# Kernel optimization log

Measured on AMD Instinct MI355X. Metric: run time of the kernel, lower is better.

## Reference

```python
import jax, jax.numpy as jnp
import numpy as np

BATCH = 8
L = 1024          # sequence length (== init arg l)
DIM = 768         # model dim
HEADS = 12
DIM_HEAD = 64
INNER = HEADS * DIM_HEAD  # 768


def setup_inputs() -> dict:
    key = jax.random.key(0)
    k1, k2, k3, k4 = jax.random.split(key, 4)
    x = jax.random.normal(k1, (BATCH, L, DIM), dtype=jnp.float32)
    # torch nn.Linear stores weight as [out_features, in_features]
    w_qkv = jax.random.normal(k2, (INNER * 3, DIM), dtype=jnp.float32) * 0.02
    w_out = jax.random.normal(k3, (DIM, INNER), dtype=jnp.float32) * 0.02
    b_out = jnp.zeros((DIM,), dtype=jnp.float32)
    # one random permutation of range(l*dim_head) per head (fixed buffers)
    perms = jnp.stack([
        jax.random.permutation(jax.random.fold_in(k4, h), L * DIM_HEAD)
        for h in range(HEADS)
    ]).astype(jnp.int32)  # [HEADS, L*DIM_HEAD]
    return {"x": x, "w_qkv": w_qkv, "w_out": w_out, "b_out": b_out, "perms": perms}


def reference(x, w_qkv, w_out, b_out, perms):
    b, n, _ = x.shape
    scale = DIM_HEAD ** -0.5
    qkv = x @ w_qkv.T                       # [b, n, 3*h*d]
    q, k, v = jnp.split(qkv, 3, axis=-1)    # each [b, n, h*d]

    def to_heads(t):
        return t.reshape(b, n, HEADS, DIM_HEAD).transpose(0, 2, 1, 3)  # [b,h,n,d]

    q, k, v = to_heads(q), to_heads(k), to_heads(v)

    # per-head permutation gather on the flattened query: flat_q[:, h] = flat_q[:, h, perm_h]
    flat_q = q.reshape(b, HEADS, n * DIM_HEAD)
    shuffled_q = jnp.take_along_axis(flat_q, perms[None, :, :], axis=2)
    sq = shuffled_q.reshape(b, HEADS, n, DIM_HEAD)

    dots = jnp.einsum('bhnd,bhmd->bhnm', sq, k) * scale  # [b,h,n,n]
    attn = jax.nn.softmax(dots, axis=-1)
    out = jnp.einsum('bhnm,bhmd->bhnd', attn, v)         # [b,h,n,d]
    out = out.transpose(0, 2, 1, 3).reshape(b, n, INNER) # [b,n,h*d]
    return out @ w_out.T + b_out                          # [b,n,dim]
```

## Files before the change

### kernel.cpp

```cpp
#include <hip/hip_runtime.h>
#include <hip/hip_bf16.h>

#define B_    8
#define L_    1024
#define DM_   768
#define H_    12
#define DH_   64
#define NQKV_ 2304
#define MTOK_ 8192
#define SCALE 0.125f
#define LDT_  72

typedef short bf16x8 __attribute__((ext_vector_type(8)));
typedef float f32x4 __attribute__((ext_vector_type(4)));

#define N_X   (MTOK_*DM_)
#define N_WQ  (NQKV_*DM_)
#define N_WO  (DM_*DM_)
#define N_CVT (N_X + N_WQ + N_WO)

static __device__ __forceinline__ unsigned short f2bu(float f) {
    unsigned int x = __float_as_uint(f);
    x = (x + 0x7fffu + ((x >> 16) & 1u)) >> 16;
    return (unsigned short)x;
}

__global__ void cvt_all_k(const float* __restrict__ x, const float* __restrict__ wq,
                          const float* __restrict__ wo,
                          unsigned short* __restrict__ xb, unsigned short* __restrict__ wqb,
                          unsigned short* __restrict__ wob) {
    int i = (blockIdx.x * blockDim.x + threadIdx.x) * 4;
    if (i >= N_CVT) return;
    const float* src; unsigned short* dst; int j = i;
    if (j < N_X)              { src = x;  dst = xb;  }
    else if ((j -= N_X) < N_WQ) { src = wq; dst = wqb; }
    else                      { j -= N_WQ; src = wo; dst = wob; }
    float4 v = *reinterpret_cast<const float4*>(src + j);
    ushort4 o;
    o.x = f2bu(v.x); o.y = f2bu(v.y); o.z = f2bu(v.z); o.w = f2bu(v.w);
    *reinterpret_cast<ushort4*>(dst + j) = o;
}

__global__ void shuffle_q_k(const unsigned short* __restrict__ Qb, const int* __restrict__ perms,
                            unsigned short* __restrict__ SQb) {
    int idx = blockIdx.x * blockDim.x + threadIdx.x;
    int i  = idx & 65535;
    int bh = idx >> 16;
    int h  = bh % H_;
    int p  = perms[h * (L_ * DH_) + i];
    SQb[(bh << 16) + i] = Qb[(bh << 16) + p];
}

static __device__ __forceinline__ int xcd_swz(int bid, int nwg) {
    int cpx = nwg >> 3;
    return (bid & 7) * cpx + (bid >> 3);
}

__global__ __launch_bounds__(256) void gemm_bt_k(
    const unsigned short* __restrict__ A,
    const unsigned short* __restrict__ Bw,
    int M, int N, int K, int mode,
    unsigned short* __restrict__ Qb, unsigned short* __restrict__ Kb, unsigned short* __restrict__ Vb,
    float* __restrict__ Cout, const float* __restrict__ bias)
{
    __shared__ __align__(16) unsigned short sA[128 * LDT_];
    __shared__ __align__(16) unsigned short sB[128 * LDT_];

    int t = threadIdx.x;
    int lane = t & 63, w = t >> 6;
    int wr = w >> 1, wc = w & 1;
    int lr = lane & 15, lg = lane >> 4;

    int nbx = N >> 7;
    int bid = xcd_swz(blockIdx.y * nbx + blockIdx.x, (M >> 7) * nbx);
    int m0 = (bid / nbx) * 128, n0 = (bid % nbx) * 128;

    f32x4 acc[4][4];
    #pragma unroll
    for (int i = 0; i < 4; ++i)
        #pragma unroll
        for (int j = 0; j < 4; ++j) acc[i][j] = (f32x4){0.f, 0.f, 0.f, 0.f};

    int r0 = t >> 3, c0 = (t & 7) * 8;

    for (int kt = 0; kt < K; kt += 64) {
        __syncthreads();
        #pragma unroll
        for (int c = 0; c < 4; ++c) {
            int row = r0 + c * 32;
            uint4 va = *reinterpret_cast<const uint4*>(A + (size_t)(m0 + row) * K + kt + c0);
            *reinterpret_cast<uint4*>(&sA[row * LDT_ + c0]) = va;
            uint4 vb = *reinterpret_cast<const uint4*>(Bw + (size_t)(n0 + row) * K + kt + c0);
            *reinterpret_cast<uint4*>(&sB[row * LDT_ + c0]) = vb;
        }
        __syncthreads();
        #pragma unroll
        for (int kk = 0; kk < 2; ++kk) {
            bf16x8 af[4], bfr[4];
            #pragma unroll
            for (int mi = 0; mi < 4; ++mi)
                af[mi] = *reinterpret_cast<const bf16x8*>(&sA[(wr*64 + mi*16 + lr) * LDT_ + kk*32 + lg*8]);
            #pragma unroll
            for (int ni = 0; ni < 4; ++ni)
                bfr[ni] = *reinterpret_cast<const bf16x8*>(&sB[(wc*64 + ni*16 + lr) * LDT_ + kk*32 + lg*8]);
            #pragma unroll
            for (int mi = 0; mi < 4; ++mi)
                #pragma unroll
                for (int ni = 0; ni < 4; ++ni)
                    acc[mi][ni] = __builtin_amdgcn_mfma_f32_16x16x32_bf16(af[mi], bfr[ni], acc[mi][ni], 0, 0, 0);
        }
    }

    if (mode == 0) {
        #pragma unroll
        for (int mi = 0; mi < 4; ++mi)
            #pragma unroll
            for (int ni = 0; ni < 4; ++ni)
                #pragma unroll
                for (int r = 0; r < 4; ++r) {
                    int gm = m0 + wr*64 + mi*16 + lg*4 + r;
                    int gc = n0 + wc*64 + ni*16 + lr;
                    int bidx = gm >> 10, tok = gm & 1023;
                    int which = gc / DM_;
                    int rem = gc - which * DM_;
                    int hh = rem >> 6, d = rem & 63;
                    unsigned short* dst = (which == 0) ? Qb : ((which == 1) ? Kb : Vb);
                    dst[(((bidx * H_ + hh) * L_) + tok) * DH_ + d] = f2bu(acc[mi][ni][r]);
                }
    } else {
        #pragma unroll
        for (int mi = 0; mi < 4; ++mi)
            #pragma unroll
            for (int ni = 0; ni < 4; ++ni)
                #pragma unroll
                for (int r = 0; r < 4; ++r) {
                    int gm = m0 + wr*64 + mi*16 + lg*4 + r;
                    int gc = n0 + wc*64 + ni*16 + lr;
                    Cout[(size_t)gm * N + gc] = acc[mi][ni][r] + bias[gc];
                }
    }
}

__global__ __launch_bounds__(256) void attn_k(
    const unsigned short* __restrict__ SQb, const unsigned short* __restrict__ Kb,
    const unsigned short* __restrict__ Vb, unsigned short* __restrict__ Ob)
{
    __shared__ __align__(16) unsigned short sQ[64 * LDT_];
    __shared__ __align__(16) unsigned short sK[64 * LDT_];
    __shared__ __align__(16) unsigned short sVT[64 * LDT_];
    __shared__ __align__(16) unsigned short sP[4][16 * LDT_];

    int t = threadIdx.x;
    int lane = t & 63, w = t >> 6;
    int lr = lane & 15, lg = lane >> 4;

    int bid = xcd_swz(blockIdx.y * gridDim.x + blockIdx.x, gridDim.x * gridDim.y);
    int bh = bid >> 4;
    int q0 = (bid & 15) * 64;
    int b = bh / H_, h = bh - b * H_;

    const unsigned short* Qp = SQb + (bh << 16);
    const unsigned short* Kp = Kb + (bh << 16);
    const unsigned short* Vp = Vb + (bh << 16);

    int r0 = t >> 3, c0 = (t & 7) * 8;
    #pragma unroll
    for (int c = 0; c < 2; ++c) {
        int row = r0 + c * 32;
        *reinterpret_cast<uint4*>(&sQ[row * LDT_ + c0]) =
            *reinterpret_cast<const uint4*>(Qp + (q0 + row) * 64 + c0);
    }

    f32x4 accO[4];
    float m_row[4], l_row[4];
    #pragma unroll
    for (int i = 0; i < 4; ++i) { accO[i] = (f32x4){0.f,0.f,0.f,0.f}; m_row[i] = -1e30f; l_row[i] = 0.f; }

    for (int kv0 = 0; kv0 < L_; kv0 += 64) {
        __syncthreads();
        #pragma unroll
        for (int c = 0; c < 2; ++c) {
            int row = r0 + c * 32;
            *reinterpret_cast<uint4*>(&sK[row * LDT_ + c0]) =
                *reinterpret_cast<const uint4*>(Kp + (kv0 + row) * 64 + c0);
            uint4 vv = *reinterpret_cast<const uint4*>(Vp + (kv0 + row) * 64 + c0);
            unsigned short tmp[8];
            *reinterpret_cast<uint4*>(tmp) = vv;
            #pragma unroll
            for (int j = 0; j < 8; ++j) sVT[(c0 + j) * LDT_ + row] = tmp[j];
        }
        __syncthreads();

        f32x4 accS[4];
        #pragma unroll
        for (int i = 0; i < 4; ++i) accS[i] = (f32x4){0.f,0.f,0.f,0.f};
        #pragma unroll
        for (int kk = 0; kk < 2; ++kk) {
            bf16x8 aq = *reinterpret_cast<const bf16x8*>(&sQ[(w*16 + lr) * LDT_ + kk*32 + lg*8]);
            #pragma unroll
            for (int nb = 0; nb < 4; ++nb) {
                bf16x8 bk = *reinterpret_cast<const bf16x8*>(&sK[(nb*16 + lr) * LDT_ + kk*32 + lg*8]);
                accS[nb] = __builtin_amdgcn_mfma_f32_16x16x32_bf16(aq, bk, accS[nb], 0, 0, 0);
            }
        }
        #pragma unroll
        for (int nb = 0; nb < 4; ++nb) accS[nb] *= SCALE;

        float mnew[4], alpha[4], rowsum[4];
        #pragma unroll
        for (int r = 0; r < 4; ++r) {
            float tm = fmaxf(fmaxf(accS[0][r], accS[1][r]), fmaxf(accS[2][r], accS[3][r]));
            #pragma unroll
            for (int off = 1; off < 16; off <<= 1) tm = fmaxf(tm, __shfl_xor(tm, off, 16));
            mnew[r]  = fmaxf(m_row[r], tm);
            alpha[r] = __expf(m_row[r] - mnew[r]);
            rowsum[r] = 0.f;
        }
        #pragma unroll
        for (int nb = 0; nb < 4; ++nb)
            #pragma unroll
            for (int r = 0; r < 4; ++r) {
                float p = __expf(accS[nb][r] - mnew[r]);
                rowsum[r] += p;
                sP[w][(lg*4 + r) * LDT_ + nb*16 + lr] = f2bu(p);
            }
        #pragma unroll
        for (int r = 0; r < 4; ++r) {
            float rs = rowsum[r];
            #pragma unroll
            for (int off = 1; off < 16; off <<= 1) rs += __shfl_xor(rs, off, 16);
            l_row[r] = l_row[r] * alpha[r] + rs;
            m_row[r] = mnew[r];
        }
        #pragma unroll
        for (int nb = 0; nb < 4; ++nb)
            #pragma unroll
            for (int r = 0; r < 4; ++r) accO[nb][r] *= alpha[r];

        __syncthreads();

        #pragma unroll
        for (int kk = 0; kk < 2; ++kk) {
            bf16x8 ap = *reinterpret_cast<const bf16x8*>(&sP[w][lr * LDT_ + kk*32 + lg*8]);
            #pragma unroll
            for (int nb = 0; nb < 4; ++nb) {
                bf16x8 bv = *reinterpret_cast<const bf16x8*>(&sVT[(nb*16 + lr) * LDT_ + kk*32 + lg*8]);
                accO[nb] = __builtin_amdgcn_mfma_f32_16x16x32_bf16(ap, bv, accO[nb], 0, 0, 0);
            }
        }
    }

    #pragma unroll
    for (int nb = 0; nb < 4; ++nb)
        #pragma unroll
        for (int r = 0; r < 4; ++r) {
            int q = q0 + w*16 + lg*4 + r;
            int d = nb*16 + lr;
            float o = accO[nb][r] / l_row[r];
            Ob[(b * L_ + q) * DM_ + h * DH_ + d] = f2bu(o);
        }
}

extern "C" void kernel_launch(void* const* d_in, const int* in_sizes, int n_in,
                              void* d_out, int out_size, void* d_ws, size_t ws_size,
                              hipStream_t stream)
{
    const float* x     = (const float*)d_in[0];
    const float* w_qkv = (const float*)d_in[1];
    const float* w_out = (const float*)d_in[2];
    const float* b_out = (const float*)d_in[3];
    const int*   perms = (const int*)d_in[4];
    float* out = (float*)d_out;

    char* ws = (char*)d_ws;
    size_t off = 0;
    auto alloc_us = [&](size_t elems) -> unsigned short* {
        unsigned short* p = (unsigned short*)(ws + off);
        off += (elems * 2 + 255) & ~(size_t)255;
        return p;
    };
    unsigned short* xb    = alloc_us((size_t)MTOK_ * DM_);
    unsigned short* wqkvb = alloc_us((size_t)NQKV_ * DM_);
    unsigned short* woutb = alloc_us((size_t)DM_ * DM_);
    unsigned short* Qb    = alloc_us((size_t)B_ * H_ * L_ * DH_);
    unsigned short* Kb2   = alloc_us((size_t)B_ * H_ * L_ * DH_);
    unsigned short* Vb2   = alloc_us((size_t)B_ * H_ * L_ * DH_);
    unsigned short* SQb   = alloc_us((size_t)B_ * H_ * L_ * DH_);
    unsigned short* Ob    = xb;

    cvt_all_k<<<(N_CVT/4 + 255)/256, 256, 0, stream>>>(x, w_qkv, w_out, xb, wqkvb, woutb);

    gemm_bt_k<<<dim3(NQKV_/128, MTOK_/128), 256, 0, stream>>>(
        xb, wqkvb, MTOK_, NQKV_, DM_, 0, Qb, Kb2, Vb2, nullptr, nullptr);

    shuffle_q_k<<<(B_*H_*L_*DH_)/256, 256, 0, stream>>>(Qb, perms, SQb);

    attn_k<<<dim3(L_/64, B_*H_), 256, 0, stream>>>(SQb, Kb2, Vb2, Ob);

    gemm_bt_k<<<dim3(DM_/128, MTOK_/128), 256, 0, stream>>>(
        Ob, woutb, MTOK_, DM_, DM_, 1, nullptr, nullptr, nullptr, out, b_out);
}
```

Before: 312.1 us.

## Use direct global-to-LDS loads with XOR swizzle, pre-transposed V, exp2 softmax

GEMM and attention tile loads now go straight from global memory into LDS through global_load_lds, and the padded LDS layout is replaced with an XOR-swizzled one to avoid bank conflicts. The QKV GEMM epilogue writes V already transposed, so attention no longer transposes V element by element in LDS. The softmax folds log2(e) into the scale and uses exp2f, and the output is normalised with a reciprocal multiply instead of a divide. The barrier before the P·V step is dropped because each wave reads only its own sP slice; the transposed V store in the epilogue is strided and may cost more global write traffic.

```diff
diff --git a/kernel.cpp b/kernel.cpp
--- a/kernel.cpp
+++ b/kernel.cpp
@@ -8,8 +8,7 @@
 #define DH_   64
 #define NQKV_ 2304
 #define MTOK_ 8192
-#define SCALE 0.125f
-#define LDT_  72
+#define SCALE2 0.1803368801f
 
 typedef short bf16x8 __attribute__((ext_vector_type(8)));
 typedef float f32x4 __attribute__((ext_vector_type(4)));
@@ -18,6 +17,10 @@
 #define N_WQ  (NQKV_*DM_)
 #define N_WO  (DM_*DM_)
 #define N_CVT (N_X + N_WQ + N_WO)
+
+#define GLDS16(gp, sp) __builtin_amdgcn_global_load_lds( \
+    (const __attribute__((address_space(1))) void*)(gp), \
+    (__attribute__((address_space(3))) void*)(sp), 16, 0, 0)
 
 static __device__ __forceinline__ unsigned short f2bu(float f) {
     unsigned int x = __float_as_uint(f);
@@ -32,9 +35,9 @@
     int i = (blockIdx.x * blockDim.x + threadIdx.x) * 4;
     if (i >= N_CVT) return;
     const float* src; unsigned short* dst; int j = i;
-    if (j < N_X)              { src = x;  dst = xb;  }
+    if (j < N_X)                { src = x;  dst = xb;  }
     else if ((j -= N_X) < N_WQ) { src = wq; dst = wqb; }
-    else                      { j -= N_WQ; src = wo; dst = wob; }
+    else                        { j -= N_WQ; src = wo; dst = wob; }
     float4 v = *reinterpret_cast<const float4*>(src + j);
     ushort4 o;
     o.x = f2bu(v.x); o.y = f2bu(v.y); o.z = f2bu(v.z); o.w = f2bu(v.w);
@@ -60,11 +63,11 @@
     const unsigned short* __restrict__ A,
     const unsigned short* __restrict__ Bw,
     int M, int N, int K, int mode,
-    unsigned short* __restrict__ Qb, unsigned short* __restrict__ Kb, unsigned short* __restrict__ Vb,
+    unsigned short* __restrict__ Qb, unsigned short* __restrict__ Kb, unsigned short* __restrict__ VTb,
     float* __restrict__ Cout, const float* __restrict__ bias)
 {
-    __shared__ __align__(16) unsigned short sA[128 * LDT_];
-    __shared__ __align__(16) unsigned short sB[128 * LDT_];
+    __shared__ __align__(16) unsigned short sA[128 * 64];
+    __shared__ __align__(16) unsigned short sB[128 * 64];
 
     int t = threadIdx.x;
     int lane = t & 63, w = t >> 6;
@@ -75,34 +78,35 @@
     int bid = xcd_swz(blockIdx.y * nbx + blockIdx.x, (M >> 7) * nbx);
     int m0 = (bid / nbx) * 128, n0 = (bid % nbx) * 128;
 
+    int srow  = lane >> 3;
+    int scol8 = ((lane & 7) ^ srow) * 8;
+
     f32x4 acc[4][4];
     #pragma unroll
     for (int i = 0; i < 4; ++i)
         #pragma unroll
         for (int j = 0; j < 4; ++j) acc[i][j] = (f32x4){0.f, 0.f, 0.f, 0.f};
 
-    int r0 = t >> 3, c0 = (t & 7) * 8;
-
     for (int kt = 0; kt < K; kt += 64) {
         __syncthreads();
         #pragma unroll
-        for (int c = 0; c < 4; ++c) {
-            int row = r0 + c * 32;
-            uint4 va = *reinterpret_cast<const uint4*>(A + (size_t)(m0 + row) * K + kt + c0);
-            *reinterpret_cast<uint4*>(&sA[row * LDT_ + c0]) = va;
-            uint4 vb = *reinterpret_cast<const uint4*>(Bw + (size_t)(n0 + row) * K + kt + c0);
-            *reinterpret_cast<uint4*>(&sB[row * LDT_ + c0]) = vb;
+        for (int i = 0; i < 4; ++i) {
+            int ch = w * 4 + i;
+            int row = ch * 8 + srow;
+            GLDS16(A  + (size_t)(m0 + row) * K + kt + scol8, sA + ch * 512);
+            GLDS16(Bw + (size_t)(n0 + row) * K + kt + scol8, sB + ch * 512);
         }
         __syncthreads();
         #pragma unroll
         for (int kk = 0; kk < 2; ++kk) {
+            int cs = ((kk * 4 + lg) ^ (lr & 7)) << 3;
             bf16x8 af[4], bfr[4];
             #pragma unroll
             for (int mi = 0; mi < 4; ++mi)
-                af[mi] = *reinterpret_cast<const bf16x8*>(&sA[(wr*64 + mi*16 + lr) * LDT_ + kk*32 + lg*8]);
+                af[mi] = *reinterpret_cast<const bf16x8*>(&sA[(wr*64 + mi*16 + lr) * 64 + cs]);
             #pragma unroll
             for (int ni = 0; ni < 4; ++ni)
-                bfr[ni] = *reinterpret_cast<const bf16x8*>(&sB[(wc*64 + ni*16 + lr) * LDT_ + kk*32 + lg*8]);
+                bfr[ni] = *reinterpret_cast<const bf16x8*>(&sB[(wc*64 + ni*16 + lr) * 64 + cs]);
             #pragma unroll
             for (int mi = 0; mi < 4; ++mi)
                 #pragma unroll
@@ -124,8 +128,10 @@
                     int which = gc / DM_;
                     int rem = gc - which * DM_;
                     int hh = rem >> 6, d = rem & 63;
-                    unsigned short* dst = (which == 0) ? Qb : ((which == 1) ? Kb : Vb);
-                    dst[(((bidx * H_ + hh) * L_) + tok) * DH_ + d] = f2bu(acc[mi][ni][r]);
+                    unsigned short v = f2bu(acc[mi][ni][r]);
+                    if (which == 0)      Qb [(((bidx * H_ + hh) * L_) + tok) * DH_ + d] = v;
+                    else if (which == 1) Kb [(((bidx * H_ + hh) * L_) + tok) * DH_ + d] = v;
+                    else                 VTb[(((bidx * H_ + hh) * DH_) + d) * L_ + tok] = v;
                 }
     } else {
         #pragma unroll
@@ -143,12 +149,12 @@
 
 __global__ __launch_bounds__(256) void attn_k(
     const unsigned short* __restrict__ SQb, const unsigned short* __restrict__ Kb,
-    const unsigned short* __restrict__ Vb, unsigned short* __restrict__ Ob)
+    const unsigned short* __restrict__ VTb, unsigned short* __restrict__ Ob)
 {
-    __shared__ __align__(16) unsigned short sQ[64 * LDT_];
-    __shared__ __align__(16) unsigned short sK[64 * LDT_];
-    __shared__ __align__(16) unsigned short sVT[64 * LDT_];
-    __shared__ __align__(16) unsigned short sP[4][16 * LDT_];
+    __shared__ __align__(16) unsigned short sQ [64 * 64];
+    __shared__ __align__(16) unsigned short sK [64 * 64];
+    __shared__ __align__(16) unsigned short sVT[64 * 64];
+    __shared__ __align__(16) unsigned short sP [4 * 16 * 64];
 
     int t = threadIdx.x;
     int lane = t & 63, w = t >> 6;
@@ -159,16 +165,18 @@
     int q0 = (bid & 15) * 64;
     int b = bh / H_, h = bh - b * H_;
 
-    const unsigned short* Qp = SQb + (bh << 16);
-    const unsigned short* Kp = Kb + (bh << 16);
-    const unsigned short* Vp = Vb + (bh << 16);
-
-    int r0 = t >> 3, c0 = (t & 7) * 8;
+    const unsigned short* Qp  = SQb + (bh << 16);
+    const unsigned short* Kp  = Kb  + (bh << 16);
+    const unsigned short* VTp = VTb + (bh << 16);
+
+    int srow  = lane >> 3;
+    int scol8 = ((lane & 7) ^ srow) * 8;
+
     #pragma unroll
-    for (int c = 0; c < 2; ++c) {
-        int row = r0 + c * 32;
-        *reinterpret_cast<uint4*>(&sQ[row * LDT_ + c0]) =
-            *reinterpret_cast<const uint4*>(Qp + (q0 + row) * 64 + c0);
+    for (int i = 0; i < 2; ++i) {
+        int ch = w * 2 + i;
+        int row = ch * 8 + srow;
+        GLDS16(Qp + (size_t)(q0 + row) * 64 + scol8, sQ + ch * 512);
     }
 
     f32x4 accO[4];
@@ -179,15 +187,11 @@
     for (int kv0 = 0; kv0 < L_; kv0 += 64) {
         __syncthreads();
         #pragma unroll
-        for (int c = 0; c < 2; ++c) {
-            int row = r0 + c * 32;
-            *reinterpret_cast<uint4*>(&sK[row * LDT_ + c0]) =
-                *reinterpret_cast<const uint4*>(Kp + (kv0 + row) * 64 + c0);
-            uint4 vv = *reinterpret_cast<const uint4*>(Vp + (kv0 + row) * 64 + c0);
-            unsigned short tmp[8];
-            *reinterpret_cast<uint4*>(tmp) = vv;
-            #pragma unroll
-            for (int j = 0; j < 8; ++j) sVT[(c0 + j) * LDT_ + row] = tmp[j];
+        for (int i = 0; i < 2; ++i) {
+            int ch = w * 2 + i;
+            int row = ch * 8 + srow;
+            GLDS16(Kp  + (size_t)(kv0 + row) * 64 + scol8, sK  + ch * 512);
+            GLDS16(VTp + (size_t)row * L_ + kv0 + scol8,   sVT + ch * 512);
         }
         __syncthreads();
 
@@ -196,15 +200,16 @@
         for (int i = 0; i < 4; ++i) accS[i] = (f32x4){0.f,0.f,0.f,0.f};
         #pragma unroll
         for (int kk = 0; kk < 2; ++kk) {
-            bf16x8 aq = *reinterpret_cast<const bf16x8*>(&sQ[(w*16 + lr) * LDT_ + kk*32 + lg*8]);
+            int cs = ((kk * 4 + lg) ^ (lr & 7)) << 3;
+            bf16x8 aq = *reinterpret_cast<const bf16x8*>(&sQ[(w*16 + lr) * 64 + cs]);
             #pragma unroll
             for (int nb = 0; nb < 4; ++nb) {
-                bf16x8 bk = *reinterpret_cast<const bf16x8*>(&sK[(nb*16 + lr) * LDT_ + kk*32 + lg*8]);
+                bf16x8 bk = *reinterpret_cast<const bf16x8*>(&sK[(nb*16 + lr) * 64 + cs]);
                 accS[nb] = __builtin_amdgcn_mfma_f32_16x16x32_bf16(aq, bk, accS[nb], 0, 0, 0);
             }
         }
         #pragma unroll
-        for (int nb = 0; nb < 4; ++nb) accS[nb] *= SCALE;
+        for (int nb = 0; nb < 4; ++nb) accS[nb] *= SCALE2;
 
         float mnew[4], alpha[4], rowsum[4];
         #pragma unroll
@@ -213,16 +218,17 @@
             #pragma unroll
             for (int off = 1; off < 16; off <<= 1) tm = fmaxf(tm, __shfl_xor(tm, off, 16));
             mnew[r]  = fmaxf(m_row[r], tm);
-            alpha[r] = __expf(m_row[r] - mnew[r]);
+            alpha[r] = exp2f(m_row[r] - mnew[r]);
             rowsum[r] = 0.f;
         }
         #pragma unroll
         for (int nb = 0; nb < 4; ++nb)
             #pragma unroll
             for (int r = 0; r < 4; ++r) {
-                float p = __expf(accS[nb][r] - mnew[r]);
+                float p = exp2f(accS[nb][r] - mnew[r]);
                 rowsum[r] += p;
-                sP[w][(lg*4 + r) * LDT_ + nb*16 + lr] = f2bu(p);
+                int prow = lg * 4 + r;
+                sP[w*1024 + prow*64 + ((((nb*2) + (lr >> 3)) ^ (prow & 7)) << 3) + (lr & 7)] = f2bu(p);
             }
         #pragma unroll
         for (int r = 0; r < 4; ++r) {
@@ -237,28 +243,28 @@
             #pragma unroll
             for (int r = 0; r < 4; ++r) accO[nb][r] *= alpha[r];
 
-        __syncthreads();
-
         #pragma unroll
         for (int kk = 0; kk < 2; ++kk) {
-            bf16x8 ap = *reinterpret_cast<const bf16x8*>(&sP[w][lr * LDT_ + kk*32 + lg*8]);
+            int cs = ((kk * 4 + lg) ^ (lr & 7)) << 3;
+            bf16x8 ap = *reinterpret_cast<const bf16x8*>(&sP[w*1024 + lr*64 + cs]);
             #pragma unroll
             for (int nb = 0; nb < 4; ++nb) {
-                bf16x8 bv = *reinterpret_cast<const bf16x8*>(&sVT[(nb*16 + lr) * LDT_ + kk*32 + lg*8]);
+                bf16x8 bv = *reinterpret_cast<const bf16x8*>(&sVT[(nb*16 + lr) * 64 + cs]);
                 accO[nb] = __builtin_amdgcn_mfma_f32_16x16x32_bf16(ap, bv, accO[nb], 0, 0, 0);
             }
         }
     }
 
     #pragma unroll
-    for (int nb = 0; nb < 4; ++nb)
-        #pragma unroll
-        for (int r = 0; r < 4; ++r) {
+    for (int r = 0; r < 4; ++r) {
+        float rinv = __builtin_amdgcn_rcpf(l_row[r]);
+        #pragma unroll
+        for (int nb = 0; nb < 4; ++nb) {
             int q = q0 + w*16 + lg*4 + r;
             int d = nb*16 + lr;
-            float o = accO[nb][r] / l_row[r];
-            Ob[(b * L_ + q) * DM_ + h * DH_ + d] = f2bu(o);
-        }
+            Ob[(b * L_ + q) * DM_ + h * DH_ + d] = f2bu(accO[nb][r] * rinv);
+        }
+    }
 }
 
 extern "C" void kernel_launch(void* const* d_in, const int* in_sizes, int n_in,
@@ -284,18 +290,18 @@
     unsigned short* woutb = alloc_us((size_t)DM_ * DM_);
     unsigned short* Qb    = alloc_us((size_t)B_ * H_ * L_ * DH_);
     unsigned short* Kb2   = alloc_us((size_t)B_ * H_ * L_ * DH_);
-    unsigned short* Vb2   = alloc_us((size_t)B_ * H_ * L_ * DH_);
+    unsigned short* VTb   = alloc_us((size_t)B_ * H_ * L_ * DH_);
     unsigned short* SQb   = alloc_us((size_t)B_ * H_ * L_ * DH_);
     unsigned short* Ob    = xb;
 
     cvt_all_k<<<(N_CVT/4 + 255)/256, 256, 0, stream>>>(x, w_qkv, w_out, xb, wqkvb, woutb);
 
     gemm_bt_k<<<dim3(NQKV_/128, MTOK_/128), 256, 0, stream>>>(
-        xb, wqkvb, MTOK_, NQKV_, DM_, 0, Qb, Kb2, Vb2, nullptr, nullptr);
+        xb, wqkvb, MTOK_, NQKV_, DM_, 0, Qb, Kb2, VTb, nullptr, nullptr);
 
     shuffle_q_k<<<(B_*H_*L_*DH_)/256, 256, 0, stream>>>(Qb, perms, SQb);
 
-    attn_k<<<dim3(L_/64, B_*H_), 256, 0, stream>>>(SQb, Kb2, Vb2, Ob);
+    attn_k<<<dim3(L_/64, B_*H_), 256, 0, stream>>>(SQb, Kb2, VTb, Ob);
 
     gemm_bt_k<<<dim3(DM_/128, MTOK_/128), 256, 0, stream>>>(
         Ob, woutb, MTOK_, DM_, DM_, 1, nullptr, nullptr, nullptr, out, b_out);
```

Result: faster. 293.3 us (-6.0%).
